# Kernel tuning notes

Measured on AMD Instinct MI355X. Metric: run time of the kernel, lower is better.

The kernel has to match this reference:

```python
import jax, jax.numpy as jnp
from jax import lax
import numpy as np
import math

DIM = 96      # channels
HEADS = 3     # num_heads
WS = 8        # window size
SHIFT = 4     # window_size // 2 (depth is odd -> shifted)
TLC = 64      # tlc_kernel
H = 264
W = 264


def _grid_idxes(h, w, k1, k2):
    # Faithful replication of the torch grids() tiling index logic (static ints).
    num_row = (h - 1) // k1 + 1
    num_col = (w - 1) // k2 + 1
    step_j = k2 if num_col == 1 else math.ceil((w - k2) / (num_col - 1) - 1e-8)
    step_i = k1 if num_row == 1 else math.ceil((h - k1) / (num_row - 1) - 1e-8)
    idxes = []
    i = 0
    last_i = False
    while i < h and not last_i:
        j = 0
        if i + k1 >= h:
            i = h - k1
            last_i = True
        last_j = False
        while j < w and not last_j:
            if j + k2 >= w:
                j = w - k2
                last_j = True
            idxes.append((i, j))
            j = j + step_j
        i = i + step_i
    return idxes


def setup_inputs() -> dict:
    key = jax.random.key(0)
    ks = jax.random.split(key, 4)
    return {
        "x": jax.random.normal(ks[0], (1, DIM, H, W), jnp.float32),
        "temperature": jnp.ones((HEADS, 1, 1), jnp.float32),
        "qkv_w": jax.random.normal(ks[1], (3 * DIM, DIM), jnp.float32) * 0.05,
        "dw_w": jax.random.normal(ks[2], (3 * DIM, 1, 3, 3), jnp.float32) * 0.1,
        "proj_w": jax.random.normal(ks[3], (DIM, DIM), jnp.float32) * 0.05,
    }


def reference(x, temperature, qkv_w, dw_w, proj_w):
    b, c, h, w = x.shape
    # depth % 2 == 1 -> cyclic shift
    x = jnp.roll(x, (-SHIFT, -SHIFT), axis=(2, 3))
    # 1x1 pointwise conv (no bias)
    qkv = jnp.einsum('oc,bchw->bohw', qkv_w, x)
    # 3x3 depthwise conv, padding 1
    qkv = lax.conv_general_dilated(
        qkv, dw_w, window_strides=(1, 1), padding=[(1, 1), (1, 1)],
        feature_group_count=3 * c, dimension_numbers=('NCHW', 'OIHW', 'NCHW'))
    # --- TLC grids: overlapping tiles (eval path, b == 1) ---
    k1, k2 = min(h, TLC), min(w, TLC)
    idxes = _grid_idxes(h, w, k1, k2)
    parts = jnp.concatenate([qkv[:, :, i:i + k1, j:j + k2] for (i, j) in idxes], axis=0)  # [T,3c,k1,k2]
    T, C3, th, tw = parts.shape
    nh, nw = th // WS, tw // WS
    # window partition: b c (h b0) (w b1) -> (b h w) c b0 b1 -> flatten spatial
    win = parts.reshape(T, C3, nh, WS, nw, WS).transpose(0, 2, 4, 1, 3, 5)
    win = win.reshape(T * nh * nw, C3, WS * WS)  # [Bw, 3c, 64]
    q, k, v = jnp.split(win, 3, axis=1)  # each [Bw, c, 64]
    ch = c // HEADS
    q = q.reshape(-1, HEADS, ch, WS * WS)
    k = k.reshape(-1, HEADS, ch, WS * WS)
    v = v.reshape(-1, HEADS, ch, WS * WS)
    # L2 normalize along token dim (F.normalize eps=1e-12)
    q = q / jnp.maximum(jnp.linalg.norm(q, axis=-1, keepdims=True), 1e-12)
    k = k / jnp.maximum(jnp.linalg.norm(k, axis=-1, keepdims=True), 1e-12)
    # channel attention: [Bw, head, ch, ch]
    attn = jax.nn.relu(jnp.einsum('bhcn,bhdn->bhcd', q, k) * temperature)
    out = jnp.einsum('bhcd,bhdn->bhcn', attn, v)  # [Bw, head, ch, 64]
    out = out.reshape(-1, c, WS, WS)
    # window merge back to tiles
    out = out.reshape(T, nh, nw, c, WS, WS).transpose(0, 3, 1, 4, 2, 5).reshape(T, c, th, tw)
    # --- TLC grids_inverse: scatter-add overlapping tiles and average ---
    preds = jnp.zeros((b, c, h, w), x.dtype)
    cnt = np.zeros((h, w), np.float32)
    for t, (i, j) in enumerate(idxes):
        preds = preds.at[0, :, i:i + k1, j:j + k2].add(out[t])
        cnt[i:i + k1, j:j + k2] += 1.0
    preds = preds / jnp.asarray(cnt)
    # 1x1 output projection
    out = jnp.einsum('oc,bchw->bohw', proj_w, preds)
    # undo cyclic shift
    return jnp.roll(out, (SHIFT, SHIFT), axis=(2, 3))
```

## Files before the change

kernel.cpp:

```cpp
#include <hip/hip_runtime.h>
#include <hip/hip_bf16.h>

#define HW_ 69696
#define W_ 264
#define H_ 264

typedef short bf16x8 __attribute__((ext_vector_type(8)));
typedef float f32x4 __attribute__((ext_vector_type(4)));

static __device__ __forceinline__ unsigned short f2b(float f) {
  __hip_bfloat16 h = __float2bfloat16(f);
  return *reinterpret_cast<unsigned short*>(&h);
}
static __device__ __forceinline__ float b2f(unsigned short u) {
  __hip_bfloat16 h;
  *reinterpret_cast<unsigned short*>(&h) = u;
  return __bfloat162float(h);
}
static __device__ __forceinline__ float lo_f(unsigned int u) {
  union { unsigned int i; float f; } c; c.i = u << 16; return c.f;
}
static __device__ __forceinline__ float hi_f(unsigned int u) {
  union { unsigned int i; float f; } c; c.i = u & 0xffff0000u; return c.f;
}

__global__ __launch_bounds__(256, 4) void k_gemm(const float* __restrict__ x,
                                                 const float* __restrict__ w,
                                                 unsigned short* __restrict__ outb) {
  __shared__ __align__(16) char smem[19968];
  unsigned short* As = (unsigned short*)smem;
  unsigned short* Cs = (unsigned short*)smem;

  const int tid = threadIdx.x;
  const int wid = tid >> 6, lane = tid & 63;
  const int quad = lane >> 4, lo = lane & 15;
  const int px0 = blockIdx.x * 64;
  const int px = px0 + wid * 16 + lo;

  const int y = px / W_, xx = px - y * W_;
  int y2 = y + 4; if (y2 >= H_) y2 -= H_;
  int x2 = xx + 4; if (x2 >= W_) x2 -= W_;
  const float* xb = x + y2 * W_ + x2;

  bf16x8 bf[3];
#pragma unroll
  for (int ks = 0; ks < 3; ++ks) {
    const float* xp = xb + (size_t)(ks * 32 + quad * 8) * HW_;
    float f[8];
#pragma unroll
    for (int i = 0; i < 8; ++i) f[i] = xp[(size_t)i * HW_];
    union { bf16x8 v; unsigned short s[8]; } u;
#pragma unroll
    for (int i = 0; i < 8; ++i) u.s[i] = f2b(f[i]);
    bf[ks] = u.v;
  }

  for (int oc = 0; oc < 3; ++oc) {
    __syncthreads();
    const float* wp = w + oc * 96 * 96;
    for (int l = tid; l < 96 * 24; l += 256) {
      int o = l / 24, c4 = (l - (l / 24) * 24) * 4;
      float4 v = *(const float4*)&wp[o * 96 + c4];
      unsigned int p0 = (unsigned int)f2b(v.x) | ((unsigned int)f2b(v.y) << 16);
      unsigned int p1 = (unsigned int)f2b(v.z) | ((unsigned int)f2b(v.w) << 16);
      *(uint2*)&As[o * 104 + c4] = make_uint2(p0, p1);
    }
    __syncthreads();

    f32x4 acc[6];
#pragma unroll
    for (int mt = 0; mt < 6; ++mt) acc[mt] = {0.f, 0.f, 0.f, 0.f};
#pragma unroll
    for (int ks = 0; ks < 3; ++ks) {
      const int kb = ks * 32 + quad * 8;
#pragma unroll
      for (int mt = 0; mt < 6; ++mt) {
        bf16x8 a = *(const bf16x8*)&As[(mt * 16 + lo) * 104 + kb];
        acc[mt] = __builtin_amdgcn_mfma_f32_16x16x32_bf16(a, bf[ks], acc[mt], 0, 0, 0);
      }
    }
    __syncthreads();

    const int pxl = wid * 16 + lo;
#pragma unroll
    for (int mt = 0; mt < 6; ++mt) {
      unsigned int p0 = (unsigned int)f2b(acc[mt][0]) | ((unsigned int)f2b(acc[mt][1]) << 16);
      unsigned int p1 = (unsigned int)f2b(acc[mt][2]) | ((unsigned int)f2b(acc[mt][3]) << 16);
      *(uint2*)&Cs[pxl * 104 + mt * 16 + quad * 4] = make_uint2(p0, p1);
    }
    __syncthreads();

    for (int i = tid; i < 64 * 12; i += 256) {
      int pxl2 = i & 63, j = i >> 6;
      *((uint4*)outb + (size_t)(oc * 12 + j) * HW_ + px0 + pxl2) =
          ((const uint4*)(Cs + pxl2 * 104))[j];
    }
  }
}

__global__ __launch_bounds__(256) void k_dw(const unsigned short* __restrict__ qkv,
                                            const float* __restrict__ dw,
                                            unsigned short* __restrict__ out) {
  __shared__ __align__(16) uint4 inS[18 * 66];
  const int tid = threadIdx.x;
  const int x0 = blockIdx.x * 64;
  const int y0 = blockIdx.y * 16;
  const int u = blockIdx.z;
  const uint4* plane = (const uint4*)qkv + (size_t)u * HW_;
  const float* wp = dw + u * 72;
  float wv[72];
#pragma unroll
  for (int i = 0; i < 72; ++i) wv[i] = wp[i];

  for (int idx = tid; idx < 18 * 66; idx += 256) {
    int rr = idx / 66, cc = idx - rr * 66;
    int gy = y0 - 1 + rr, gx = x0 - 1 + cc;
    uint4 v = make_uint4(0u, 0u, 0u, 0u);
    if ((unsigned)gy < (unsigned)H_ && (unsigned)gx < (unsigned)W_)
      v = plane[gy * W_ + gx];
    inS[idx] = v;
  }
  __syncthreads();

#pragma unroll
  for (int k = 0; k < 4; ++k) {
    const int oidx = k * 256 + tid;
    const int ro = oidx >> 6, co = oidx & 63;
    const int y = y0 + ro, x = x0 + co;
    float acc[8] = {0.f, 0.f, 0.f, 0.f, 0.f, 0.f, 0.f, 0.f};
#pragma unroll
    for (int dy = 0; dy < 3; ++dy)
#pragma unroll
      for (int dx = 0; dx < 3; ++dx) {
        uint4 v = inS[(ro + dy) * 66 + co + dx];
        float w0 = wv[0 * 9 + dy * 3 + dx], w1 = wv[1 * 9 + dy * 3 + dx];
        float w2 = wv[2 * 9 + dy * 3 + dx], w3 = wv[3 * 9 + dy * 3 + dx];
        float w4 = wv[4 * 9 + dy * 3 + dx], w5 = wv[5 * 9 + dy * 3 + dx];
        float w6 = wv[6 * 9 + dy * 3 + dx], w7 = wv[7 * 9 + dy * 3 + dx];
        acc[0] += w0 * lo_f(v.x); acc[1] += w1 * hi_f(v.x);
        acc[2] += w2 * lo_f(v.y); acc[3] += w3 * hi_f(v.y);
        acc[4] += w4 * lo_f(v.z); acc[5] += w5 * hi_f(v.z);
        acc[6] += w6 * lo_f(v.w); acc[7] += w7 * hi_f(v.w);
      }
    if (y < H_ && x < W_) {
      uint4 o;
      o.x = (unsigned int)f2b(acc[0]) | ((unsigned int)f2b(acc[1]) << 16);
      o.y = (unsigned int)f2b(acc[2]) | ((unsigned int)f2b(acc[3]) << 16);
      o.z = (unsigned int)f2b(acc[4]) | ((unsigned int)f2b(acc[5]) << 16);
      o.w = (unsigned int)f2b(acc[6]) | ((unsigned int)f2b(acc[7]) << 16);
      *((uint4*)out + (size_t)u * HW_ + y * W_ + x) = o;
    }
  }
}

#define P1 200
#define P8 1608
__global__ __launch_bounds__(192) void k_attn(const unsigned short* __restrict__ qd,
                                              const float* __restrict__ temp,
                                              unsigned short* __restrict__ tout) {
  __shared__ __align__(16) unsigned short flat[8 * P8];
  __shared__ __align__(16) unsigned short attnL[3 * 32 * 40];
  __shared__ float invn[3 * 32];
  const int tid = threadIdx.x;
  const int wi = blockIdx.x, t = blockIdx.y;
  const int i0 = (t / 5) * 50, j0 = (t % 5) * 50;
  const int wy = wi >> 3, wx = wi & 7;
  const int gy0 = i0 + wy * 8, gx0 = j0 + wx * 8;

  {
    const size_t base = (size_t)gy0 * W_ + gx0;
    for (int idx = tid; idx < 24 * 64; idx += 192) {
      int u = idx >> 6, rj = idx & 63, r = rj >> 3, j = rj & 7;
      uint4 v = ((const uint4*)qd)[(size_t)u * HW_ + base + r * W_ + j];
      ((uint4*)flat)[r * 201 + j * 25 + u] = v;
    }
  }
  __syncthreads();

  const int h = tid >> 6, lane = tid & 63;
  const int quad = lane >> 4, lo = lane & 15;
  const int cb = h * 32;

  bf16x8 qf[2][2], kf[2][2];
#pragma unroll
  for (int mt = 0; mt < 2; ++mt)
#pragma unroll
    for (int kt = 0; kt < 2; ++kt) {
      const int rbase = (kt * 4 + quad) * P8;
      const int cq = cb + mt * 16 + lo;
      const int ck = 96 + cb + mt * 16 + lo;
      bf16x8 q8, k8;
#pragma unroll
      for (int j = 0; j < 8; ++j) {
        q8[j] = (short)flat[rbase + j * P1 + cq];
        k8[j] = (short)flat[rbase + j * P1 + ck];
      }
      qf[mt][kt] = q8;
      kf[mt][kt] = k8;
    }

  f32x4 S[2][2];
#pragma unroll
  for (int mt = 0; mt < 2; ++mt)
#pragma unroll
    for (int nt = 0; nt < 2; ++nt) {
      S[mt][nt] = {0.f, 0.f, 0.f, 0.f};
#pragma unroll
      for (int kt = 0; kt < 2; ++kt)
        S[mt][nt] = __builtin_amdgcn_mfma_f32_16x16x32_bf16(qf[mt][kt], kf[nt][kt], S[mt][nt], 0, 0, 0);
    }

  float ivk[2];
#pragma unroll
  for (int mt = 0; mt < 2; ++mt) {
    float sq = 0.f, sk = 0.f;
#pragma unroll
    for (int kt = 0; kt < 2; ++kt)
#pragma unroll
      for (int j = 0; j < 8; ++j) {
        float a = b2f((unsigned short)qf[mt][kt][j]);
        float b = b2f((unsigned short)kf[mt][kt][j]);
        sq += a * a;
        sk += b * b;
      }
    sq += __shfl_xor(sq, 16);
    sq += __shfl_xor(sq, 32);
    sk += __shfl_xor(sk, 16);
    sk += __shfl_xor(sk, 32);
    if (quad == 0) invn[h * 32 + mt * 16 + lo] = 1.f / fmaxf(sqrtf(sq), 1e-12f);
    ivk[mt] = 1.f / fmaxf(sqrtf(sk), 1e-12f);
  }
  __syncthreads();

  const float ts = temp[h];
#pragma unroll
  for (int mt = 0; mt < 2; ++mt)
#pragma unroll
    for (int nt = 0; nt < 2; ++nt)
#pragma unroll
      for (int r = 0; r < 4; ++r) {
        int c = mt * 16 + quad * 4 + r;
        float v = S[mt][nt][r] * invn[h * 32 + c] * ivk[nt] * ts;
        attnL[(h * 32 + c) * 40 + nt * 16 + lo] = f2b(fmaxf(v, 0.f));
      }
  __syncthreads();

  bf16x8 af[2];
#pragma unroll
  for (int mt = 0; mt < 2; ++mt)
    af[mt] = *(const bf16x8*)&attnL[(h * 32 + mt * 16 + lo) * 40 + quad * 8];

  const int uv = 24 + h * 4 + quad;
  f32x4 O[2][4];
#pragma unroll
  for (int nt = 0; nt < 4; ++nt) {
    const int px = nt * 16 + lo;
    const size_t gpx = (size_t)(gy0 + (px >> 3)) * W_ + gx0 + (px & 7);
    uint4 vraw = ((const uint4*)qd)[(size_t)uv * HW_ + gpx];
    bf16x8 vf = *reinterpret_cast<bf16x8*>(&vraw);
#pragma unroll
    for (int mt = 0; mt < 2; ++mt) {
      f32x4 z = {0.f, 0.f, 0.f, 0.f};
      O[mt][nt] = __builtin_amdgcn_mfma_f32_16x16x32_bf16(af[mt], vf, z, 0, 0, 0);
    }
  }
  __syncthreads();

  unsigned short* Cs = flat;
#pragma unroll
  for (int mt = 0; mt < 2; ++mt)
#pragma unroll
    for (int nt = 0; nt < 4; ++nt) {
      const int px = nt * 16 + lo;
      unsigned int p0 = (unsigned int)f2b(O[mt][nt][0]) | ((unsigned int)f2b(O[mt][nt][1]) << 16);
      unsigned int p1 = (unsigned int)f2b(O[mt][nt][2]) | ((unsigned int)f2b(O[mt][nt][3]) << 16);
      *(uint2*)&Cs[px * 104 + cb + mt * 16 + quad * 4] = make_uint2(p0, p1);
    }
  __syncthreads();

  for (int idx = tid; idx < 64 * 12; idx += 192) {
    int rec = idx / 12, u = idx - (idx / 12) * 12;
    int r = rec >> 3, j = rec & 7;
    size_t g = (size_t)t * 4096 + (wy * 8 + r) * 64 + wx * 8 + j;
    ((uint4*)tout)[g * 12 + u] = ((const uint4*)(Cs + rec * 104))[u];
  }
}

__global__ __launch_bounds__(256, 4) void k_avgproj(const float* __restrict__ w,
                                                    const unsigned short* __restrict__ tout,
                                                    float* __restrict__ outf) {
  __shared__ __align__(16) unsigned short As[96 * 104];
  const int tid = threadIdx.x;
  const int wid = tid >> 6, lane = tid & 63;
  const int quad = lane >> 4, lo = lane & 15;
  const int px0 = blockIdx.x * 64;
  const int px = px0 + wid * 16 + lo;

  for (int l = tid; l < 96 * 24; l += 256) {
    int o = l / 24, c4 = (l - (l / 24) * 24) * 4;
    float4 v = *(const float4*)&w[o * 96 + c4];
    unsigned int p0 = (unsigned int)f2b(v.x) | ((unsigned int)f2b(v.y) << 16);
    unsigned int p1 = (unsigned int)f2b(v.z) | ((unsigned int)f2b(v.w) << 16);
    *(uint2*)&As[o * 104 + c4] = make_uint2(p0, p1);
  }

  const int y = px / W_, xx = px - y * W_;
  int loy = (y >= 64) ? (y - 14) / 50 : 0;
  int hiy = y / 50; if (hiy > 4) hiy = 4;
  int lox = (xx >= 64) ? (xx - 14) / 50 : 0;
  int hix = xx / 50; if (hix > 4) hix = 4;
  float a24[24];
#pragma unroll
  for (int i = 0; i < 24; ++i) a24[i] = 0.f;
  int cnt = 0;
  for (int ty = loy; ty <= hiy; ++ty)
    for (int tx = lox; tx <= hix; ++tx) {
      size_t rec = (size_t)(ty * 5 + tx) * 4096 + ((y - ty * 50) << 6) + (xx - tx * 50);
      const uint4* rp = (const uint4*)tout + rec * 12 + quad;
#pragma unroll
      for (int ks = 0; ks < 3; ++ks) {
        uint4 v = rp[ks * 4];
        a24[ks * 8 + 0] += lo_f(v.x); a24[ks * 8 + 1] += hi_f(v.x);
        a24[ks * 8 + 2] += lo_f(v.y); a24[ks * 8 + 3] += hi_f(v.y);
        a24[ks * 8 + 4] += lo_f(v.z); a24[ks * 8 + 5] += hi_f(v.z);
        a24[ks * 8 + 6] += lo_f(v.w); a24[ks * 8 + 7] += hi_f(v.w);
      }
      ++cnt;
    }
  const float inv = 1.f / (float)cnt;
  bf16x8 bf[3];
#pragma unroll
  for (int ks = 0; ks < 3; ++ks) {
    union { bf16x8 v; unsigned short s[8]; } u;
#pragma unroll
    for (int i = 0; i < 8; ++i) u.s[i] = f2b(a24[ks * 8 + i] * inv);
    bf[ks] = u.v;
  }
  __syncthreads();

  f32x4 acc[6];
#pragma unroll
  for (int mt = 0; mt < 6; ++mt) acc[mt] = {0.f, 0.f, 0.f, 0.f};
#pragma unroll
  for (int ks = 0; ks < 3; ++ks) {
    const int kb = ks * 32 + quad * 8;
#pragma unroll
    for (int mt = 0; mt < 6; ++mt) {
      bf16x8 a = *(const bf16x8*)&As[(mt * 16 + lo) * 104 + kb];
      acc[mt] = __builtin_amdgcn_mfma_f32_16x16x32_bf16(a, bf[ks], acc[mt], 0, 0, 0);
    }
  }

  {
    int y2 = y + 4; if (y2 >= H_) y2 -= H_;
    int x2 = xx + 4; if (x2 >= W_) x2 -= W_;
    int tp = y2 * W_ + x2;
#pragma unroll
    for (int mt = 0; mt < 6; ++mt) {
      int row = mt * 16 + quad * 4;
#pragma unroll
      for (int r = 0; r < 4; ++r)
        outf[(size_t)(row + r) * HW_ + tp] = acc[mt][r];
    }
  }
}

extern "C" void kernel_launch(void* const* d_in, const int* in_sizes, int n_in,
                              void* d_out, int out_size, void* d_ws, size_t ws_size,
                              hipStream_t stream) {
  (void)in_sizes; (void)n_in; (void)out_size; (void)ws_size;
  const float* x = (const float*)d_in[0];
  const float* temp = (const float*)d_in[1];
  const float* qkvw = (const float*)d_in[2];
  const float* dww = (const float*)d_in[3];
  const float* projw = (const float*)d_in[4];
  float* out = (float*)d_out;

  char* ws = (char*)d_ws;
  const size_t SZQ = (size_t)288 * HW_ * 2;
  unsigned short* qkvb = (unsigned short*)ws;
  unsigned short* tout = (unsigned short*)ws;
  unsigned short* qkvd = (unsigned short*)(ws + SZQ);

  k_gemm<<<dim3(1089), 256, 0, stream>>>(x, qkvw, qkvb);
  k_dw<<<dim3(5, 17, 36), 256, 0, stream>>>(qkvb, dww, qkvd);
  k_attn<<<dim3(64, 25), 192, 0, stream>>>(qkvd, temp, tout);
  k_avgproj<<<dim3(1089), 256, 0, stream>>>(projw, tout, out);
}
```

Baseline: 150.7 us.

## Fuse depthwise conv into per-window attention kernel, dropping intermediate qkv buffer

Merges the depthwise 3x3 conv and the window attention into one kernel. Each block loads a 10x10 halo per channel group from the pointwise-conv output, computes the depthwise conv into shared memory, then runs the attention from shared memory. This removes the write and re-read of the full depthwise output buffer and one launch. In exchange it recomputes halo pixels for overlapping tiles and windows, and one of the four waves idles during the attention phase.

```diff
diff --git a/kernel.cpp b/kernel.cpp
--- a/kernel.cpp
+++ b/kernel.cpp
@@ -98,187 +98,187 @@
   }
 }
 
-__global__ __launch_bounds__(256) void k_dw(const unsigned short* __restrict__ qkv,
-                                            const float* __restrict__ dw,
-                                            unsigned short* __restrict__ out) {
-  __shared__ __align__(16) uint4 inS[18 * 66];
+__global__ __launch_bounds__(256, 3) void k_dwattn(const unsigned short* __restrict__ qkvb,
+                                                   const float* __restrict__ dwv,
+                                                   const float* __restrict__ temp,
+                                                   unsigned short* __restrict__ tout) {
+  __shared__ __align__(16) unsigned short outS[64 * 296];
+  __shared__ __align__(16) uint4 stg[4][100];
+  __shared__ __align__(16) unsigned short attnL[3 * 32 * 40];
+  __shared__ float invn[3 * 32];
+
   const int tid = threadIdx.x;
-  const int x0 = blockIdx.x * 64;
-  const int y0 = blockIdx.y * 16;
-  const int u = blockIdx.z;
-  const uint4* plane = (const uint4*)qkv + (size_t)u * HW_;
-  const float* wp = dw + u * 72;
-  float wv[72];
-#pragma unroll
-  for (int i = 0; i < 72; ++i) wv[i] = wp[i];
-
-  for (int idx = tid; idx < 18 * 66; idx += 256) {
-    int rr = idx / 66, cc = idx - rr * 66;
-    int gy = y0 - 1 + rr, gx = x0 - 1 + cc;
-    uint4 v = make_uint4(0u, 0u, 0u, 0u);
-    if ((unsigned)gy < (unsigned)H_ && (unsigned)gx < (unsigned)W_)
-      v = plane[gy * W_ + gx];
-    inS[idx] = v;
-  }
-  __syncthreads();
-
-#pragma unroll
-  for (int k = 0; k < 4; ++k) {
-    const int oidx = k * 256 + tid;
-    const int ro = oidx >> 6, co = oidx & 63;
-    const int y = y0 + ro, x = x0 + co;
-    float acc[8] = {0.f, 0.f, 0.f, 0.f, 0.f, 0.f, 0.f, 0.f};
-#pragma unroll
-    for (int dy = 0; dy < 3; ++dy)
-#pragma unroll
-      for (int dx = 0; dx < 3; ++dx) {
-        uint4 v = inS[(ro + dy) * 66 + co + dx];
-        float w0 = wv[0 * 9 + dy * 3 + dx], w1 = wv[1 * 9 + dy * 3 + dx];
-        float w2 = wv[2 * 9 + dy * 3 + dx], w3 = wv[3 * 9 + dy * 3 + dx];
-        float w4 = wv[4 * 9 + dy * 3 + dx], w5 = wv[5 * 9 + dy * 3 + dx];
-        float w6 = wv[6 * 9 + dy * 3 + dx], w7 = wv[7 * 9 + dy * 3 + dx];
-        acc[0] += w0 * lo_f(v.x); acc[1] += w1 * hi_f(v.x);
-        acc[2] += w2 * lo_f(v.y); acc[3] += w3 * hi_f(v.y);
-        acc[4] += w4 * lo_f(v.z); acc[5] += w5 * hi_f(v.z);
-        acc[6] += w6 * lo_f(v.w); acc[7] += w7 * hi_f(v.w);
-      }
-    if (y < H_ && x < W_) {
+  const int wi = ((blockIdx.x & 7) << 3) | (blockIdx.x >> 3);
+  const int t = blockIdx.y;
+  const int i0 = (t / 5) * 50, j0 = (t % 5) * 50;
+  const int wy = wi >> 3, wx = wi & 7;
+  const int gy0 = i0 + wy * 8, gx0 = j0 + wx * 8;
+
+  const int h = tid >> 6, lane = tid & 63;
+  const int w_ = __builtin_amdgcn_readfirstlane(h);
+
+  {
+    uint4* stgW = &stg[w_][0];
+    const int r0 = lane >> 3, c0 = lane & 7;
+    const int sy0 = lane / 10, sx0 = lane - sy0 * 10;
+    const int ii1 = lane + 64;
+    const int sy1 = ii1 / 10, sx1 = ii1 - sy1 * 10;
+    const int gyA = gy0 - 1 + sy0, gxA = gx0 - 1 + sx0;
+    const int gyB = gy0 - 1 + sy1, gxB = gx0 - 1 + sx1;
+    const bool okA = (unsigned)gyA < (unsigned)H_ && (unsigned)gxA < (unsigned)W_;
+    const bool okB = ii1 < 100 && (unsigned)gyB < (unsigned)H_ && (unsigned)gxB < (unsigned)W_;
+    const size_t offA = (size_t)gyA * W_ + gxA;
+    const size_t offB = (size_t)gyB * W_ + gxB;
+    const uint4* qb4 = (const uint4*)qkvb;
+
+    uint4 vA = okA ? qb4[(size_t)w_ * HW_ + offA] : make_uint4(0u, 0u, 0u, 0u);
+    uint4 vB = okB ? qb4[(size_t)w_ * HW_ + offB] : make_uint4(0u, 0u, 0u, 0u);
+
+    for (int k = 0; k < 9; ++k) {
+      const int u = k * 4 + w_;
+      stgW[lane] = vA;
+      if (ii1 < 100) stgW[ii1] = vB;
+      if (k < 8) {
+        vA = okA ? qb4[(size_t)(u + 4) * HW_ + offA] : make_uint4(0u, 0u, 0u, 0u);
+        vB = okB ? qb4[(size_t)(u + 4) * HW_ + offB] : make_uint4(0u, 0u, 0u, 0u);
+      }
+      asm volatile("s_waitcnt lgkmcnt(0)" ::: "memory");
+      __builtin_amdgcn_sched_barrier(0);
+
+      const float* wp = dwv + u * 72;
+      float acc[8] = {0.f, 0.f, 0.f, 0.f, 0.f, 0.f, 0.f, 0.f};
+#pragma unroll
+      for (int dy = 0; dy < 3; ++dy)
+#pragma unroll
+        for (int dx = 0; dx < 3; ++dx) {
+          uint4 v = stgW[(r0 + dy) * 10 + (c0 + dx)];
+          float w0 = wp[0 * 9 + dy * 3 + dx], w1 = wp[1 * 9 + dy * 3 + dx];
+          float w2 = wp[2 * 9 + dy * 3 + dx], w3 = wp[3 * 9 + dy * 3 + dx];
+          float w4 = wp[4 * 9 + dy * 3 + dx], w5 = wp[5 * 9 + dy * 3 + dx];
+          float w6 = wp[6 * 9 + dy * 3 + dx], w7 = wp[7 * 9 + dy * 3 + dx];
+          acc[0] += w0 * lo_f(v.x); acc[1] += w1 * hi_f(v.x);
+          acc[2] += w2 * lo_f(v.y); acc[3] += w3 * hi_f(v.y);
+          acc[4] += w4 * lo_f(v.z); acc[5] += w5 * hi_f(v.z);
+          acc[6] += w6 * lo_f(v.w); acc[7] += w7 * hi_f(v.w);
+        }
       uint4 o;
       o.x = (unsigned int)f2b(acc[0]) | ((unsigned int)f2b(acc[1]) << 16);
       o.y = (unsigned int)f2b(acc[2]) | ((unsigned int)f2b(acc[3]) << 16);
       o.z = (unsigned int)f2b(acc[4]) | ((unsigned int)f2b(acc[5]) << 16);
       o.w = (unsigned int)f2b(acc[6]) | ((unsigned int)f2b(acc[7]) << 16);
-      *((uint4*)out + (size_t)u * HW_ + y * W_ + x) = o;
-    }
-  }
-}
-
-#define P1 200
-#define P8 1608
-__global__ __launch_bounds__(192) void k_attn(const unsigned short* __restrict__ qd,
-                                              const float* __restrict__ temp,
-                                              unsigned short* __restrict__ tout) {
-  __shared__ __align__(16) unsigned short flat[8 * P8];
-  __shared__ __align__(16) unsigned short attnL[3 * 32 * 40];
-  __shared__ float invn[3 * 32];
-  const int tid = threadIdx.x;
-  const int wi = blockIdx.x, t = blockIdx.y;
-  const int i0 = (t / 5) * 50, j0 = (t % 5) * 50;
-  const int wy = wi >> 3, wx = wi & 7;
-  const int gy0 = i0 + wy * 8, gx0 = j0 + wx * 8;
-
-  {
-    const size_t base = (size_t)gy0 * W_ + gx0;
-    for (int idx = tid; idx < 24 * 64; idx += 192) {
-      int u = idx >> 6, rj = idx & 63, r = rj >> 3, j = rj & 7;
-      uint4 v = ((const uint4*)qd)[(size_t)u * HW_ + base + r * W_ + j];
-      ((uint4*)flat)[r * 201 + j * 25 + u] = v;
-    }
-  }
-  __syncthreads();
-
-  const int h = tid >> 6, lane = tid & 63;
+      *(uint4*)&outS[lane * 296 + u * 8] = o;
+    }
+  }
+  __syncthreads();
+
   const int quad = lane >> 4, lo = lane & 15;
   const int cb = h * 32;
 
   bf16x8 qf[2][2], kf[2][2];
-#pragma unroll
-  for (int mt = 0; mt < 2; ++mt)
-#pragma unroll
-    for (int kt = 0; kt < 2; ++kt) {
-      const int rbase = (kt * 4 + quad) * P8;
-      const int cq = cb + mt * 16 + lo;
-      const int ck = 96 + cb + mt * 16 + lo;
-      bf16x8 q8, k8;
-#pragma unroll
-      for (int j = 0; j < 8; ++j) {
-        q8[j] = (short)flat[rbase + j * P1 + cq];
-        k8[j] = (short)flat[rbase + j * P1 + ck];
-      }
-      qf[mt][kt] = q8;
-      kf[mt][kt] = k8;
-    }
-
   f32x4 S[2][2];
-#pragma unroll
-  for (int mt = 0; mt < 2; ++mt)
-#pragma unroll
-    for (int nt = 0; nt < 2; ++nt) {
-      S[mt][nt] = {0.f, 0.f, 0.f, 0.f};
+  float ivk[2];
+  if (h < 3) {
+#pragma unroll
+    for (int mt = 0; mt < 2; ++mt)
+#pragma unroll
+      for (int kt = 0; kt < 2; ++kt) {
+        const int rr = kt * 4 + quad;
+        const int cq = cb + mt * 16 + lo;
+        const int ck = 96 + cq;
+        bf16x8 q8, k8;
+#pragma unroll
+        for (int j = 0; j < 8; ++j) {
+          q8[j] = (short)outS[(rr * 8 + j) * 296 + cq];
+          k8[j] = (short)outS[(rr * 8 + j) * 296 + ck];
+        }
+        qf[mt][kt] = q8;
+        kf[mt][kt] = k8;
+      }
+
+#pragma unroll
+    for (int mt = 0; mt < 2; ++mt)
+#pragma unroll
+      for (int nt = 0; nt < 2; ++nt) {
+        S[mt][nt] = {0.f, 0.f, 0.f, 0.f};
+#pragma unroll
+        for (int kt = 0; kt < 2; ++kt)
+          S[mt][nt] = __builtin_amdgcn_mfma_f32_16x16x32_bf16(qf[mt][kt], kf[nt][kt], S[mt][nt], 0, 0, 0);
+      }
+
+#pragma unroll
+    for (int mt = 0; mt < 2; ++mt) {
+      float sq = 0.f, sk = 0.f;
 #pragma unroll
       for (int kt = 0; kt < 2; ++kt)
-        S[mt][nt] = __builtin_amdgcn_mfma_f32_16x16x32_bf16(qf[mt][kt], kf[nt][kt], S[mt][nt], 0, 0, 0);
-    }
-
-  float ivk[2];
-#pragma unroll
-  for (int mt = 0; mt < 2; ++mt) {
-    float sq = 0.f, sk = 0.f;
-#pragma unroll
-    for (int kt = 0; kt < 2; ++kt)
-#pragma unroll
-      for (int j = 0; j < 8; ++j) {
-        float a = b2f((unsigned short)qf[mt][kt][j]);
-        float b = b2f((unsigned short)kf[mt][kt][j]);
-        sq += a * a;
-        sk += b * b;
-      }
-    sq += __shfl_xor(sq, 16);
-    sq += __shfl_xor(sq, 32);
-    sk += __shfl_xor(sk, 16);
-    sk += __shfl_xor(sk, 32);
-    if (quad == 0) invn[h * 32 + mt * 16 + lo] = 1.f / fmaxf(sqrtf(sq), 1e-12f);
-    ivk[mt] = 1.f / fmaxf(sqrtf(sk), 1e-12f);
-  }
-  __syncthreads();
-
-  const float ts = temp[h];
-#pragma unroll
-  for (int mt = 0; mt < 2; ++mt)
-#pragma unroll
-    for (int nt = 0; nt < 2; ++nt)
-#pragma unroll
-      for (int r = 0; r < 4; ++r) {
-        int c = mt * 16 + quad * 4 + r;
-        float v = S[mt][nt][r] * invn[h * 32 + c] * ivk[nt] * ts;
-        attnL[(h * 32 + c) * 40 + nt * 16 + lo] = f2b(fmaxf(v, 0.f));
-      }
-  __syncthreads();
-
-  bf16x8 af[2];
-#pragma unroll
-  for (int mt = 0; mt < 2; ++mt)
-    af[mt] = *(const bf16x8*)&attnL[(h * 32 + mt * 16 + lo) * 40 + quad * 8];
-
-  const int uv = 24 + h * 4 + quad;
+#pragma unroll
+        for (int j = 0; j < 8; ++j) {
+          float a = b2f((unsigned short)qf[mt][kt][j]);
+          float b = b2f((unsigned short)kf[mt][kt][j]);
+          sq += a * a;
+          sk += b * b;
+        }
+      sq += __shfl_xor(sq, 16);
+      sq += __shfl_xor(sq, 32);
+      sk += __shfl_xor(sk, 16);
+      sk += __shfl_xor(sk, 32);
+      if (quad == 0) invn[h * 32 + mt * 16 + lo] = 1.f / fmaxf(sqrtf(sq), 1e-12f);
+      ivk[mt] = 1.f / fmaxf(sqrtf(sk), 1e-12f);
+    }
+  }
+  __syncthreads();
+
+  if (h < 3) {
+    const float ts = temp[h];
+#pragma unroll
+    for (int mt = 0; mt < 2; ++mt)
+#pragma unroll
+      for (int nt = 0; nt < 2; ++nt)
+#pragma unroll
+        for (int r = 0; r < 4; ++r) {
+          int c = mt * 16 + quad * 4 + r;
+          float v = S[mt][nt][r] * invn[h * 32 + c] * ivk[nt] * ts;
+          attnL[(h * 32 + c) * 40 + nt * 16 + lo] = f2b(fmaxf(v, 0.f));
+        }
+  }
+  __syncthreads();
+
   f32x4 O[2][4];
-#pragma unroll
-  for (int nt = 0; nt < 4; ++nt) {
-    const int px = nt * 16 + lo;
-    const size_t gpx = (size_t)(gy0 + (px >> 3)) * W_ + gx0 + (px & 7);
-    uint4 vraw = ((const uint4*)qd)[(size_t)uv * HW_ + gpx];
-    bf16x8 vf = *reinterpret_cast<bf16x8*>(&vraw);
-#pragma unroll
-    for (int mt = 0; mt < 2; ++mt) {
-      f32x4 z = {0.f, 0.f, 0.f, 0.f};
-      O[mt][nt] = __builtin_amdgcn_mfma_f32_16x16x32_bf16(af[mt], vf, z, 0, 0, 0);
-    }
-  }
-  __syncthreads();
-
-  unsigned short* Cs = flat;
-#pragma unroll
-  for (int mt = 0; mt < 2; ++mt)
+  if (h < 3) {
+    bf16x8 af[2];
+#pragma unroll
+    for (int mt = 0; mt < 2; ++mt)
+      af[mt] = *(const bf16x8*)&attnL[(h * 32 + mt * 16 + lo) * 40 + quad * 8];
+
+    const int uv = 24 + h * 4 + quad;
 #pragma unroll
     for (int nt = 0; nt < 4; ++nt) {
       const int px = nt * 16 + lo;
-      unsigned int p0 = (unsigned int)f2b(O[mt][nt][0]) | ((unsigned int)f2b(O[mt][nt][1]) << 16);
-      unsigned int p1 = (unsigned int)f2b(O[mt][nt][2]) | ((unsigned int)f2b(O[mt][nt][3]) << 16);
-      *(uint2*)&Cs[px * 104 + cb + mt * 16 + quad * 4] = make_uint2(p0, p1);
-    }
-  __syncthreads();
-
-  for (int idx = tid; idx < 64 * 12; idx += 192) {
+      uint4 vraw = *(const uint4*)&outS[px * 296 + uv * 8];
+      bf16x8 vf = *reinterpret_cast<bf16x8*>(&vraw);
+#pragma unroll
+      for (int mt = 0; mt < 2; ++mt) {
+        f32x4 z = {0.f, 0.f, 0.f, 0.f};
+        O[mt][nt] = __builtin_amdgcn_mfma_f32_16x16x32_bf16(af[mt], vf, z, 0, 0, 0);
+      }
+    }
+  }
+  __syncthreads();
+
+  unsigned short* Cs = outS;
+  if (h < 3) {
+#pragma unroll
+    for (int mt = 0; mt < 2; ++mt)
+#pragma unroll
+      for (int nt = 0; nt < 4; ++nt) {
+        const int px = nt * 16 + lo;
+        unsigned int p0 = (unsigned int)f2b(O[mt][nt][0]) | ((unsigned int)f2b(O[mt][nt][1]) << 16);
+        unsigned int p1 = (unsigned int)f2b(O[mt][nt][2]) | ((unsigned int)f2b(O[mt][nt][3]) << 16);
+        *(uint2*)&Cs[px * 104 + cb + mt * 16 + quad * 4] = make_uint2(p0, p1);
+      }
+  }
+  __syncthreads();
+
+  for (int idx = tid; idx < 64 * 12; idx += 256) {
     int rec = idx / 12, u = idx - (idx / 12) * 12;
     int r = rec >> 3, j = rec & 7;
     size_t g = (size_t)t * 4096 + (wy * 8 + r) * 64 + wx * 8 + j;
@@ -379,11 +379,9 @@
   char* ws = (char*)d_ws;
   const size_t SZQ = (size_t)288 * HW_ * 2;
   unsigned short* qkvb = (unsigned short*)ws;
-  unsigned short* tout = (unsigned short*)ws;
-  unsigned short* qkvd = (unsigned short*)(ws + SZQ);
+  unsigned short* tout = (unsigned short*)(ws + SZQ);
 
   k_gemm<<<dim3(1089), 256, 0, stream>>>(x, qkvw, qkvb);
-  k_dw<<<dim3(5, 17, 36), 256, 0, stream>>>(qkvb, dww, qkvd);
-  k_attn<<<dim3(64, 25), 192, 0, stream>>>(qkvd, temp, tout);
+  k_dwattn<<<dim3(64, 25), 256, 0, stream>>>(qkvb, dww, temp, tout);
   k_avgproj<<<dim3(1089), 256, 0, stream>>>(projw, tout, out);
 }
```

Measured after the change: 142.8 us. -5.2%, faster.
